# Kernel tuning notes

Hardware: AMD Instinct MI355X
Metric: run time of the kernel (lower is better)

Reference implementation:

```python
import jax, jax.numpy as jnp
import numpy as np

DIM = 512
HEADS = 8
DIM_HEAD = 64
INNER = HEADS * DIM_HEAD  # 512
B, N = 32, 512
LN_EPS = 1e-5


def setup_inputs() -> dict:
    key = jax.random.key(0)
    ks = jax.random.split(key, 8)
    inp = {
        "q": jax.random.normal(ks[0], (B, N, DIM), jnp.float32),
        "k": jax.random.normal(ks[1], (B, N, DIM), jnp.float32),
        "v": jax.random.normal(ks[2], (B, N, DIM), jnp.float32),
        "ln_w": jnp.ones((DIM,), jnp.float32),
        "ln_b": jnp.zeros((DIM,), jnp.float32),
        "W_in": jax.random.normal(ks[3], (DIM, INNER), jnp.float32) / np.sqrt(DIM),
        "W_out": jax.random.normal(ks[4], (INNER, DIM), jnp.float32) / np.sqrt(INNER),
        "b_out": jnp.zeros((DIM,), jnp.float32),
        "cov_w_raw": jnp.float32(0.6),
        "var_w_raw": jnp.float32(0.2),
    }
    return inp


def _project(x, ln_w, ln_b, W_in):
    # LayerNorm(dim) -> Linear(dim, inner, bias=False) -> 'b n (h d) -> h b n d'
    mu = jnp.mean(x, axis=-1, keepdims=True)
    var = jnp.var(x, axis=-1, keepdims=True)  # biased, as in nn.LayerNorm
    xn = (x - mu) / jnp.sqrt(var + LN_EPS) * ln_w + ln_b
    f = xn @ W_in  # [B, N, inner]
    Bq, Nq, _ = f.shape
    f = f.reshape(Bq, Nq, HEADS, DIM_HEAD)
    return jnp.transpose(f, (2, 0, 1, 3))  # [h, B, N, d]


def reference(q, k, v, ln_w, ln_b, W_in, W_out, b_out, cov_w_raw, var_w_raw):
    f_q = _project(q, ln_w, ln_b, W_in)  # [h, B, N, d]
    f_k = _project(k, ln_w, ln_b, W_in)
    f_v = _project(v, ln_w, ln_b, W_in)

    d = f_q.shape[-1]

    # cosine similarity: (q . k) / (||q|| ||k||)
    dots = jnp.einsum('hbnd,hbmd->hbnm', f_q, f_k)
    qn = jnp.linalg.norm(f_q, axis=-1)  # [h, B, N]
    kn = jnp.linalg.norm(f_k, axis=-1)  # [h, B, M]
    cosine_sim = dots / (qn[..., :, None] * kn[..., None, :])

    # basic covariance component: centered dot / d
    qc = f_q - jnp.mean(f_q, axis=-1, keepdims=True)
    kc = f_k - jnp.mean(f_k, axis=-1, keepdims=True)
    cov_component = jnp.einsum('hbnd,hbmd->hbnm', qc, kc) / d

    # variance component: outer product of per-token variances (unbiased) / d
    q_var = jnp.var(f_q, axis=-1, ddof=1)  # [h, B, N]
    k_var = jnp.var(f_k, axis=-1, ddof=1)  # [h, B, M]
    var_component = (q_var[..., :, None] * k_var[..., None, :]) / d

    cov_w = jax.nn.sigmoid(cov_w_raw)
    var_w = jax.nn.sigmoid(var_w_raw)
    cos_w = 1.0 - cov_w - var_w

    scores = cos_w * cosine_sim + cov_w * cov_component + var_w * var_component
    out = jnp.einsum('hbnm,hbmd->hbnd', scores, f_v)  # no softmax in cosine variant

    # 'h b n d -> b n (h d)'
    out = jnp.transpose(out, (1, 2, 0, 3)).reshape(out.shape[1], out.shape[2], INNER)
    return out @ W_out + b_out
```

## Files before the change

kernel.cpp:

```cpp
#include <hip/hip_runtime.h>
#include <stdint.h>

using u16 = unsigned short;
using u32 = unsigned int;
using bf16x8 = __bf16 __attribute__((ext_vector_type(8)));
using f32x4  = float __attribute__((ext_vector_type(4)));

__device__ __forceinline__ float bflo(u32 u){ return __uint_as_float(u << 16); }
__device__ __forceinline__ float bfhi(u32 u){ return __uint_as_float(u & 0xffff0000u); }
__device__ __forceinline__ u16 f2bf(float f){
  u32 u = __float_as_uint(f);
  u += 0x7fffu + ((u >> 16) & 1u);
  return (u16)(u >> 16);
}
__device__ __forceinline__ u32 pk2(float a, float b){
  return (u32)f2bf(a) | ((u32)f2bf(b) << 16);
}
__device__ __forceinline__ void gload16(const void* g, void* l){
  __builtin_amdgcn_global_load_lds(
      (const __attribute__((address_space(1))) void*)(uintptr_t)(g),
      (__attribute__((address_space(3))) void*)(uintptr_t)(l), 16, 0, 0);
}

__global__ __launch_bounds__(256) void prep_k(const float* __restrict__ Win,
                                              const float* __restrict__ Wout,
                                              const float* __restrict__ lnw,
                                              const float* __restrict__ lnb,
                                              u16* __restrict__ WpT,
                                              u16* __restrict__ WoutT,
                                              float* __restrict__ g1,
                                              float* __restrict__ g2){
  __shared__ float tile[32][33];
  __shared__ float red[2][8][32];
  int bid = blockIdx.x;
  if (bid < 512){
    int bz = bid >> 8, bi = bid & 255;
    int bx = bi & 15, by = bi >> 4;
    const float* src = bz ? Wout : Win;
    u16* dst = bz ? WoutT : WpT;
    int tx = threadIdx.x & 31, ty = threadIdx.x >> 5;
    int c0 = bx * 32, r0 = by * 32;
#pragma unroll
    for (int i = 0; i < 4; ++i)
      tile[ty + i*8][tx] = src[(size_t)(r0 + ty + i*8)*512 + c0 + tx];
    __syncthreads();
    float sc = bz ? 1.f : lnw[r0 + tx];
#pragma unroll
    for (int i = 0; i < 4; ++i)
      dst[(size_t)(c0 + ty + i*8)*512 + r0 + tx] = f2bf(tile[tx][ty + i*8] * sc);
  } else {
    int bi = bid - 512;
    int col = bi*32 + (threadIdx.x & 31);
    int s = threadIdx.x >> 5;
    float p1 = 0.f, p2 = 0.f;
    for (int kk = 0; kk < 64; ++kk){
      int k = s*64 + kk;
      float wv = Win[(size_t)k*512 + col];
      p1 += lnw[k]*wv; p2 += lnb[k]*wv;
    }
    red[0][s][threadIdx.x & 31] = p1;
    red[1][s][threadIdx.x & 31] = p2;
    __syncthreads();
    if (threadIdx.x < 32){
      float a1 = 0.f, a2 = 0.f;
#pragma unroll
      for (int s2 = 0; s2 < 8; ++s2){ a1 += red[0][s2][threadIdx.x]; a2 += red[1][s2][threadIdx.x]; }
      g1[bi*32 + threadIdx.x] = a1;
      g2[bi*32 + threadIdx.x] = a2;
    }
  }
}

template<int ORIENT, int FSTAT>
__device__ __forceinline__ void proj_body(
    const float* __restrict__ X, const u16* __restrict__ Wp,
    const float* __restrict__ g1, const float* __restrict__ g2,
    u16* __restrict__ C, float* __restrict__ fstat, int ldC, int bid,
    char* sW, char* sX, float* sF){
  float* sMu = sF;        float* sRs = sF + 128;
  float* sG1 = sF + 256;  float* sG2 = sF + 384;
  const int t = threadIdx.x, w = t >> 6, l = t & 63;
  const int wr = w >> 1, wc = w & 1;
  const int lr = l & 15, lg = l >> 4;
  int bx, by;
  if (ORIENT == 0){ bx = bid & 127; by = bid >> 7; }
  else { int j = bid >> 3; bx = j & 3; by = (bid & 7) + 8*(j >> 2); }
  const int row0 = bx * 128, col0 = by * 128;
  const int xbase = (ORIENT == 0) ? row0 : col0;
  const int wbase = (ORIENT == 0) ? col0 : row0;

  const int sc = t >> 3, k8 = t & 7;
  const int sso = (k8*16) ^ ((sc & 7) << 4);
  const char* Wpp = (const char*)Wp + ((size_t)(wbase + sc) << 10) + sso;
  const float* Xp = X + ((size_t)(xbase + sc) << 9) + k8*8;

  if (t < 128){ sG1[t] = g1[wbase + t]; sG2[t] = g2[wbase + t]; }

  float psum[4] = {}, pss[4] = {};
  f32x4 acc[4][4] = {};

  for (int kt = 0; kt < 8; ++kt){
    __syncthreads();
#pragma unroll
    for (int ii = 0; ii < 4; ++ii){
      gload16(Wpp + (size_t)ii*32768 + kt*128, sW + ii*4096 + w*1024);
      const float* p = Xp + ii*(32*512) + kt*64;
      float4 a = *(const float4*)p, c4 = *(const float4*)(p + 4);
      psum[ii] += ((a.x+a.y)+(a.z+a.w)) + ((c4.x+c4.y)+(c4.z+c4.w));
      pss[ii]  += ((a.x*a.x+a.y*a.y)+(a.z*a.z+a.w*a.w))
                + ((c4.x*c4.x+c4.y*c4.y)+(c4.z*c4.z+c4.w*c4.w));
      uint4 pk;
      pk.x = pk2(a.x,  a.y);  pk.y = pk2(a.z,  a.w);
      pk.z = pk2(c4.x, c4.y); pk.w = pk2(c4.z, c4.w);
      *(uint4*)(sX + (sc + ii*32)*128 + sso) = pk;
    }
    __syncthreads();
    const char* aB = (ORIENT == 0) ? sX : sW;
    const char* bB = (ORIENT == 0) ? sW : sX;
#pragma unroll
    for (int kk = 0; kk < 2; ++kk){
      bf16x8 af[4], bfg[4];
#pragma unroll
      for (int m = 0; m < 4; ++m){
        int r = wr*64 + m*16 + lr;
        af[m] = *(const bf16x8*)(aB + r*128 + ((kk*64 + lg*16) ^ ((r & 7) << 4)));
      }
#pragma unroll
      for (int n = 0; n < 4; ++n){
        int r = wc*64 + n*16 + lr;
        bfg[n] = *(const bf16x8*)(bB + r*128 + ((kk*64 + lg*16) ^ ((r & 7) << 4)));
      }
#pragma unroll
      for (int m = 0; m < 4; ++m)
#pragma unroll
        for (int n = 0; n < 4; ++n)
          acc[m][n] = __builtin_amdgcn_mfma_f32_16x16x32_bf16(af[m], bfg[n], acc[m][n], 0, 0, 0);
    }
  }

#pragma unroll
  for (int ii = 0; ii < 4; ++ii){
    float s = psum[ii], s2 = pss[ii];
#pragma unroll
    for (int off = 1; off < 8; off <<= 1){ s += __shfl_xor(s, off); s2 += __shfl_xor(s2, off); }
    if (k8 == 0){
      float mu = s * (1.f/512.f);
      sMu[sc + ii*32] = mu;
      sRs[sc + ii*32] = rsqrtf(s2 * (1.f/512.f) - mu*mu + 1e-5f);
    }
  }
  __syncthreads();

  float cs[4] = {}, cs2[4] = {};
#pragma unroll
  for (int m = 0; m < 4; ++m){
#pragma unroll
    for (int q = 0; q < 4; ++q){
      int ri = wr*64 + m*16 + lg*4 + q;
      float rsv = 0.f, muv = 0.f, g1r = 0.f, g2r = 0.f;
      if (ORIENT == 0){ rsv = sRs[ri]; muv = sMu[ri]; }
      else { g1r = sG1[ri]; g2r = sG2[ri]; }
      float fv[4];
#pragma unroll
      for (int n = 0; n < 4; ++n){
        int ci = wc*64 + n*16 + lr;
        float a = acc[m][n][q];
        if (ORIENT == 0) fv[n] = rsv*(a - muv*sG1[ci]) + sG2[ci];
        else             fv[n] = sRs[ci]*(a - sMu[ci]*g1r) + g2r;
        C[(size_t)(row0 + ri)*ldC + (col0 + ci)] = f2bf(fv[n]);
        if (FSTAT == 2){ cs[n] += fv[n]; cs2[n] += fv[n]*fv[n]; }
      }
      if (FSTAT == 1){
        float s  = (fv[0]+fv[1]) + (fv[2]+fv[3]);
        float s2 = (fv[0]*fv[0]+fv[1]*fv[1]) + (fv[2]*fv[2]+fv[3]*fv[3]);
#pragma unroll
        for (int off = 1; off < 16; off <<= 1){ s += __shfl_xor(s, off); s2 += __shfl_xor(s2, off); }
        if (lr == 0){
          int head = (col0 >> 6) + wc;
          *(float2*)(fstat + ((size_t)(row0 + ri)*8 + head)*2) = make_float2(s, s2);
        }
      }
    }
  }
  if (FSTAT == 2){
    int head = (row0 >> 6) + wr;
#pragma unroll
    for (int n = 0; n < 4; ++n){
      float s = cs[n], s2 = cs2[n];
      s += __shfl_xor(s, 16); s2 += __shfl_xor(s2, 16);
      s += __shfl_xor(s, 32); s2 += __shfl_xor(s2, 32);
      if (lg == 0){
        int tok = col0 + wc*64 + n*16 + lr;
        *(float2*)(fstat + ((size_t)tok*8 + head)*2) = make_float2(s, s2);
      }
    }
  }
}

__global__ __launch_bounds__(256, 4) void proj_k(
    const float* __restrict__ q, const float* __restrict__ k, const float* __restrict__ v,
    const u16* __restrict__ Wp, const float* __restrict__ g1, const float* __restrict__ g2,
    u16* __restrict__ fq, u16* __restrict__ kT, u16* __restrict__ vT,
    float* __restrict__ qstat, float* __restrict__ kstat){
  __shared__ __align__(16) char sW[16384];
  __shared__ __align__(16) char sX[16384];
  __shared__ float sF[512];
  int bid = blockIdx.x;
  if (bid < 512)
    proj_body<0,1>(q, Wp, g1, g2, fq, qstat, 512, bid, sW, sX, sF);
  else if (bid < 1024)
    proj_body<1,2>(k, Wp, g1, g2, kT, kstat, 16384, bid - 512, sW, sX, sF);
  else
    proj_body<1,0>(v, Wp, g1, g2, vT, nullptr, 16384, bid - 1024, sW, sX, sF);
}

__global__ __launch_bounds__(256) void outgemm_k(
    const u16* __restrict__ A, const u16* __restrict__ B,
    float* __restrict__ Cf, const float* __restrict__ bias){
  __shared__ __align__(16) char sA[16384];
  __shared__ __align__(16) char sB[16384];
  const int t = threadIdx.x, w = t >> 6, l = t & 63;
  const int wr = w >> 1, wc = w & 1;
  const int lr = l & 15, lg = l >> 4;
  const int row0 = blockIdx.x * 128, col0 = blockIdx.y * 128;
  f32x4 acc[4][4] = {};

  const int sc = t >> 3, k8 = t & 7;
  const int sso = (k8*16) ^ ((sc & 7) << 4);
  const char* Ap = (const char*)A + ((size_t)(row0 + sc) << 10) + sso;
  const char* Bp = (const char*)B + ((size_t)(col0 + sc) << 10) + sso;

  for (int kt = 0; kt < 8; ++kt){
    __syncthreads();
#pragma unroll
    for (int ii = 0; ii < 4; ++ii){
      gload16(Ap + (size_t)ii*32768 + kt*128, sA + ii*4096 + w*1024);
      gload16(Bp + (size_t)ii*32768 + kt*128, sB + ii*4096 + w*1024);
    }
    __syncthreads();
#pragma unroll
    for (int kk = 0; kk < 2; ++kk){
      bf16x8 af[4], bfg[4];
#pragma unroll
      for (int m = 0; m < 4; ++m){
        int r = wr*64 + m*16 + lr;
        af[m] = *(const bf16x8*)(sA + r*128 + ((kk*64 + lg*16) ^ ((r & 7) << 4)));
      }
#pragma unroll
      for (int n = 0; n < 4; ++n){
        int r = wc*64 + n*16 + lr;
        bfg[n] = *(const bf16x8*)(sB + r*128 + ((kk*64 + lg*16) ^ ((r & 7) << 4)));
      }
#pragma unroll
      for (int m = 0; m < 4; ++m)
#pragma unroll
        for (int n = 0; n < 4; ++n)
          acc[m][n] = __builtin_amdgcn_mfma_f32_16x16x32_bf16(af[m], bfg[n], acc[m][n], 0, 0, 0);
    }
  }
#pragma unroll
  for (int m = 0; m < 4; ++m){
#pragma unroll
    for (int q = 0; q < 4; ++q){
      int r = row0 + wr*64 + m*16 + lg*4 + q;
#pragma unroll
      for (int n = 0; n < 4; ++n){
        int cc = col0 + wc*64 + n*16 + lr;
        Cf[(size_t)r*512 + cc] = acc[m][n][q] + bias[cc];
      }
    }
  }
}

__global__ __launch_bounds__(512) void attn_k(
    const u16* __restrict__ fq, const u16* __restrict__ kT, const u16* __restrict__ vT,
    const float* __restrict__ qstat, const float* __restrict__ kstat,
    u16* __restrict__ ao,
    const float* __restrict__ cwr, const float* __restrict__ vwr){
  __shared__ __align__(16) char smem[131072 + 1664*4];
  float* sStat = (float*)(smem + 131072);
  float* sS1 = sStat + 1536;
  float* sS2 = sStat + 1600;

  const int t = threadIdx.x, w = t >> 6, l = t & 63;
  const int lr = l & 15, lg = l >> 4;
  const int h = blockIdx.x & 7, b = blockIdx.x >> 3;

  float cwv = 1.f/(1.f + __expf(-*cwr));
  float vwv = 1.f/(1.f + __expf(-*vwr));
  float cosw = 1.f - cwv - vwv;

  const char* kTb = (const char*)kT + (size_t)h*64*32768 + (size_t)b*1024;
  const char* vTb = (const char*)vT + (size_t)h*64*32768 + (size_t)b*1024;
#pragma unroll
  for (int ii = 0; ii < 8; ++ii){
    int c = ii*512 + t, d = c >> 6, u = c & 63;
    int so = d*32768 + ((u ^ (d & 7)) << 4);
    gload16(kTb + so, smem + ii*8192 + w*1024);
    gload16(vTb + so, smem + 65536 + ii*8192 + w*1024);
  }
  {
    float2 ksr = *(const float2*)(kstat + ((size_t)(b*512 + t)*8 + h)*2);
    float mk = ksr.x * (1.f/64.f);
    sStat[t]        = rsqrtf(ksr.y);
    sStat[512 + t]  = mk;
    sStat[1024 + t] = (ksr.y - 64.f*mk*mk) * (1.f/63.f);
  }
  __syncthreads();

  const int jt = (w >> 1), itp = (w & 1);
  f32x4 m2acc[2] = {}, m1acc[2] = {};
  {
    const int j = jt*16 + lr;
#pragma unroll
    for (int ks = 0; ks < 16; ++ks){
      int u = ks*4 + lg;
      bf16x8 af = *(const bf16x8*)(smem + 65536 + j*1024 + ((u ^ (j & 7)) << 4));
#pragma unroll
      for (int tt = 0; tt < 2; ++tt){
        int i = (itp*2 + tt)*16 + lr;
        bf16x8 bf = *(const bf16x8*)(smem + i*1024 + ((u ^ (i & 7)) << 4));
        m2acc[tt] = __builtin_amdgcn_mfma_f32_16x16x32_bf16(af, bf, m2acc[tt], 0, 0, 0);
      }
    }
  }
  {
    int j = t >> 3, g = t & 7;
    float p1 = 0.f, p2 = 0.f;
#pragma unroll
    for (int uu = 0; uu < 8; ++uu){
      int ut = g*8 + uu;
      uint4 uv = *(const uint4*)(smem + 65536 + j*1024 + ((ut ^ (j & 7)) << 4));
      int m0 = ut*8;
      float4 mk0 = *(const float4*)(sStat + 512 + m0);
      float4 mk1 = *(const float4*)(sStat + 512 + m0 + 4);
      float4 kv0 = *(const float4*)(sStat + 1024 + m0);
      float4 kv1 = *(const float4*)(sStat + 1024 + m0 + 4);
      float v0=bflo(uv.x),v1=bfhi(uv.x),v2=bflo(uv.y),v3=bfhi(uv.y);
      float v4=bflo(uv.z),v5=bfhi(uv.z),v6=bflo(uv.w),v7=bfhi(uv.w);
      p1 += v0*mk0.x + v1*mk0.y + v2*mk0.z + v3*mk0.w
          + v4*mk1.x + v5*mk1.y + v6*mk1.z + v7*mk1.w;
      p2 += v0*kv0.x + v1*kv0.y + v2*kv0.z + v3*kv0.w
          + v4*kv1.x + v5*kv1.y + v6*kv1.z + v7*kv1.w;
    }
#pragma unroll
    for (int off = 1; off < 8; off <<= 1){ p1 += __shfl_xor(p1, off); p2 += __shfl_xor(p2, off); }
    if (g == 0){ sS1[j] = p1; sS2[j] = p2; }
  }
  __syncthreads();

#pragma unroll
  for (int ii = 0; ii < 32; ++ii){
    int wd = ii*512 + t;
    int d = wd >> 8, o = wd & 255, ud = o >> 2, p = o & 3;
    int m0 = ((ud ^ (d & 7)) << 3) + p*2;
    u32 uv = *(u32*)(smem + wd*4);
    *(u32*)(smem + wd*4) = pk2(bflo(uv)*sStat[m0], bfhi(uv)*sStat[m0+1]);
  }
  __syncthreads();

  {
    const int j = jt*16 + lr;
#pragma unroll
    for (int ks = 0; ks < 16; ++ks){
      int u = ks*4 + lg;
      bf16x8 af = *(const bf16x8*)(smem + 65536 + j*1024 + ((u ^ (j & 7)) << 4));
#pragma unroll
      for (int tt = 0; tt < 2; ++tt){
        int i = (itp*2 + tt)*16 + lr;
        bf16x8 bf = *(const bf16x8*)(smem + i*1024 + ((u ^ (i & 7)) << 4));
        m1acc[tt] = __builtin_amdgcn_mfma_f32_16x16x32_bf16(af, bf, m1acc[tt], 0, 0, 0);
      }
    }
  }
  __syncthreads();

#pragma unroll
  for (int tt = 0; tt < 2; ++tt){
#pragma unroll
    for (int q = 0; q < 4; ++q){
      int j = jt*16 + lg*4 + q;
      int i = (itp*2 + tt)*16 + lr;
      int bo = j*128 + (((i >> 3) ^ (j & 7)) << 4) + (i & 7)*2;
      *(u16*)(smem + bo)        = f2bf(m1acc[tt][q]);
      *(u16*)(smem + 8192 + bo) = f2bf(m2acc[tt][q]);
    }
  }
  const char* fqb = (const char*)fq + (size_t)b*524288 + h*128;
#pragma unroll
  for (int ii = 0; ii < 8; ++ii){
    int c = ii*512 + t, n = c >> 3, u = c & 7;
    gload16(fqb + n*1024 + ((u ^ (n & 7)) << 4), smem + 65536 + ii*8192 + w*1024);
  }
  __syncthreads();

  float s1v[4], s2v[4];
#pragma unroll
  for (int nt = 0; nt < 4; ++nt){ s1v[nt] = sS1[nt*16 + lr]; s2v[nt] = sS2[nt*16 + lr]; }
  const float Bc = cwv * (1.f/64.f);

#pragma unroll
  for (int mt = 0; mt < 4; ++mt){
    f32x4 a1[4] = {}, a2[4] = {};
    const int n = w*64 + mt*16 + lr;
#pragma unroll
    for (int kk = 0; kk < 2; ++kk){
      int u = kk*4 + lg;
      bf16x8 af = *(const bf16x8*)(smem + 65536 + n*128 + ((u ^ (n & 7)) << 4));
#pragma unroll
      for (int nt = 0; nt < 4; ++nt){
        int j = nt*16 + lr;
        bf16x8 b1 = *(const bf16x8*)(smem + j*128 + ((u ^ (j & 7)) << 4));
        bf16x8 b2 = *(const bf16x8*)(smem + 8192 + j*128 + ((u ^ (j & 7)) << 4));
        a1[nt] = __builtin_amdgcn_mfma_f32_16x16x32_bf16(af, b1, a1[nt], 0, 0, 0);
        a2[nt] = __builtin_amdgcn_mfma_f32_16x16x32_bf16(af, b2, a2[nt], 0, 0, 0);
      }
    }
#pragma unroll
    for (int q = 0; q < 4; ++q){
      int nr = w*64 + mt*16 + lg*4 + q;
      float2 qs = *(const float2*)(qstat + ((size_t)(b*512 + nr)*8 + h)*2);
      float mq = qs.x * (1.f/64.f);
      float An = cosw * rsqrtf(qs.y);
      float Cn = -cwv * mq;
      float En = vwv * (1.f/64.f) * ((qs.y - 64.f*mq*mq) * (1.f/63.f));
      char* op = (char*)ao + ((size_t)(b*512 + nr)*512 + h*64)*2;
#pragma unroll
      for (int nt = 0; nt < 4; ++nt){
        float ov = An*a1[nt][q] + Bc*a2[nt][q] + Cn*s1v[nt] + En*s2v[nt];
        *(u16*)(op + (nt*16 + lr)*2) = f2bf(ov);
      }
    }
  }
}

extern "C" void kernel_launch(void* const* d_in, const int* in_sizes, int n_in,
                              void* d_out, int out_size, void* d_ws, size_t ws_size,
                              hipStream_t stream){
  const float* q    = (const float*)d_in[0];
  const float* k    = (const float*)d_in[1];
  const float* v    = (const float*)d_in[2];
  const float* lnw  = (const float*)d_in[3];
  const float* lnb  = (const float*)d_in[4];
  const float* Win  = (const float*)d_in[5];
  const float* Wout = (const float*)d_in[6];
  const float* bout = (const float*)d_in[7];
  const float* cwr  = (const float*)d_in[8];
  const float* vwr  = (const float*)d_in[9];

  char* ws = (char*)d_ws;
  const size_t FB = (size_t)16384 * 512 * 2;
  u16* fq  = (u16*)(ws);
  u16* kT  = (u16*)(ws + FB);
  u16* vT  = (u16*)(ws + 2*FB);
  u16* ao  = (u16*)(ws + 3*FB);
  u16* WpT   = (u16*)(ws + 4*FB);
  u16* WoutT = (u16*)(ws + 4*FB + 524288);
  float* g1  = (float*)(ws + 4*FB + 1048576);
  float* g2  = (float*)(ws + 4*FB + 1048576 + 2048);
  float* qstat = (float*)d_out;
  float* kstat = qstat + 262144;

  prep_k<<<528, 256, 0, stream>>>(Win, Wout, lnw, lnb, WpT, WoutT, g1, g2);

  proj_k<<<1536, 256, 0, stream>>>(q, k, v, WpT, g1, g2, fq, kT, vT, qstat, kstat);

  attn_k<<<256, 512, 0, stream>>>(fq, kT, vT, qstat, kstat, ao, cwr, vwr);

  outgemm_k<<<dim3(128,4), 256, 0, stream>>>(ao, WoutT, (float*)d_out, bout);
}
```

Baseline: 105.8 us.

## Prefetch next X tile into registers during MFMA in projection GEMM

```diff
diff --git a/kernel.cpp b/kernel.cpp
--- a/kernel.cpp
+++ b/kernel.cpp
@@ -96,25 +96,45 @@
 
   if (t < 128){ sG1[t] = g1[wbase + t]; sG2[t] = g2[wbase + t]; }
 
+  float xr[4][8];
   float psum[4] = {}, pss[4] = {};
   f32x4 acc[4][4] = {};
 
-  for (int kt = 0; kt < 8; ++kt){
-    __syncthreads();
+  auto XLOAD = [&](int kt){
 #pragma unroll
     for (int ii = 0; ii < 4; ++ii){
-      gload16(Wpp + (size_t)ii*32768 + kt*128, sW + ii*4096 + w*1024);
       const float* p = Xp + ii*(32*512) + kt*64;
       float4 a = *(const float4*)p, c4 = *(const float4*)(p + 4);
-      psum[ii] += ((a.x+a.y)+(a.z+a.w)) + ((c4.x+c4.y)+(c4.z+c4.w));
-      pss[ii]  += ((a.x*a.x+a.y*a.y)+(a.z*a.z+a.w*a.w))
-                + ((c4.x*c4.x+c4.y*c4.y)+(c4.z*c4.z+c4.w*c4.w));
+      xr[ii][0]=a.x;  xr[ii][1]=a.y;  xr[ii][2]=a.z;  xr[ii][3]=a.w;
+      xr[ii][4]=c4.x; xr[ii][5]=c4.y; xr[ii][6]=c4.z; xr[ii][7]=c4.w;
+    }
+  };
+  auto XWRITE = [&](){
+#pragma unroll
+    for (int ii = 0; ii < 4; ++ii){
+#pragma unroll
+      for (int e = 0; e < 8; ++e){ psum[ii] += xr[ii][e]; pss[ii] += xr[ii][e]*xr[ii][e]; }
       uint4 pk;
-      pk.x = pk2(a.x,  a.y);  pk.y = pk2(a.z,  a.w);
-      pk.z = pk2(c4.x, c4.y); pk.w = pk2(c4.z, c4.w);
+      pk.x = pk2(xr[ii][0], xr[ii][1]); pk.y = pk2(xr[ii][2], xr[ii][3]);
+      pk.z = pk2(xr[ii][4], xr[ii][5]); pk.w = pk2(xr[ii][6], xr[ii][7]);
       *(uint4*)(sX + (sc + ii*32)*128 + sso) = pk;
     }
-    __syncthreads();
+  };
+  auto WSTAGE = [&](int kt){
+#pragma unroll
+    for (int ii = 0; ii < 4; ++ii)
+      gload16(Wpp + (size_t)ii*32768 + kt*128, sW + ii*4096 + w*1024);
+  };
+
+  XLOAD(0);
+  for (int kt = 0; kt < 8; ++kt){
+    WSTAGE(kt);
+    XWRITE();
+    asm volatile("s_waitcnt vmcnt(0) lgkmcnt(0)" ::: "memory");
+    __builtin_amdgcn_s_barrier();
+    __builtin_amdgcn_sched_barrier(0);
+    if (kt < 7) XLOAD(kt + 1);
+    __builtin_amdgcn_sched_barrier(0);
     const char* aB = (ORIENT == 0) ? sX : sW;
     const char* bB = (ORIENT == 0) ? sW : sX;
 #pragma unroll
@@ -136,6 +156,9 @@
         for (int n = 0; n < 4; ++n)
           acc[m][n] = __builtin_amdgcn_mfma_f32_16x16x32_bf16(af[m], bfg[n], acc[m][n], 0, 0, 0);
     }
+    asm volatile("s_waitcnt lgkmcnt(0)" ::: "memory");
+    __builtin_amdgcn_s_barrier();
+    __builtin_amdgcn_sched_barrier(0);
   }
 
 #pragma unroll
@@ -197,7 +220,7 @@
   }
 }
 
-__global__ __launch_bounds__(256, 4) void proj_k(
+__global__ __launch_bounds__(256, 3) void proj_k(
     const float* __restrict__ q, const float* __restrict__ k, const float* __restrict__ v,
     const u16* __restrict__ Wp, const float* __restrict__ g1, const float* __restrict__ g2,
     u16* __restrict__ fq, u16* __restrict__ kT, u16* __restrict__ vT,
```

After: 98.89 us. 6.5% less time.
